# Kernel optimization log

Hardware: AMD Instinct MI355X
Metric: run time of the kernel (lower is better)

The kernel has to match this reference:

```python
import jax, jax.numpy as jnp
import numpy as np

P = 32            # patch_num_row
KS = 5            # kernel_size
DIM = 1024
HEADS = 16
DIM_HEAD = 64
INNER = HEADS * DIM_HEAD
SCALE = DIM_HEAD ** -0.5


def _nearby_mask(p=P, ks=KS):
    # True = masked out (matches torch masked_fill semantics)
    pad = ks // 2
    m = np.ones((p * p, p + 2 * pad, p + 2 * pad), dtype=bool)
    for i in range(p):
        for j in range(p):
            m[i * p + j, i:i + ks, j:j + ks] = False
    m = m[:, pad:-pad, pad:-pad].reshape(p * p, p * p)
    # F.pad(mask, (1,0,1,0), value=False): unmasked first row/col (BOS token)
    m = np.pad(m, ((1, 0), (1, 0)), constant_values=False)
    return jnp.asarray(m)  # [n, n], n = p*p + 1

NB_MASK = _nearby_mask()


def setup_inputs() -> dict:
    key = jax.random.key(0)
    ks = jax.random.split(key, 8)
    b, n = 16, P * P + 1
    s = DIM ** -0.5
    return {
        "q": jax.random.normal(ks[0], (b, n, DIM), jnp.float32),
        "k": jax.random.normal(ks[1], (b, n, DIM), jnp.float32),
        "v": jax.random.normal(ks[2], (b, n, DIM), jnp.float32),
        "Wq": jax.random.normal(ks[3], (DIM, INNER), jnp.float32) * s,
        "Wk": jax.random.normal(ks[4], (DIM, INNER), jnp.float32) * s,
        "Wv": jax.random.normal(ks[5], (DIM, INNER), jnp.float32) * s,
        "Wo": jax.random.normal(ks[6], (INNER, DIM), jnp.float32) * (INNER ** -0.5),
        "bo": jnp.zeros((DIM,), jnp.float32),
    }


def reference(q, k, v, Wq, Wk, Wv, Wo, bo):
    b, n, _ = q.shape
    h, d = HEADS, DIM_HEAD
    # projections, split heads: b n (h d) -> b h n d
    qh = (q @ Wq).reshape(b, n, h, d).transpose(0, 2, 1, 3)
    kh = (k @ Wk).reshape(b, n, h, d).transpose(0, 2, 1, 3)
    vh = (v @ Wv).reshape(b, n, h, d).transpose(0, 2, 1, 3)
    dots = jnp.einsum('bhid,bhjd->bhij', qh, kh) * SCALE
    mask_value = -jnp.finfo(dots.dtype).max
    dots = jnp.where(NB_MASK[None, None], mask_value, dots)
    attn = jax.nn.softmax(dots, axis=-1)
    out = jnp.einsum('bhij,bhjd->bhid', attn, vh)
    out = out.transpose(0, 2, 1, 3).reshape(b, n, h * d)
    return out @ Wo + bo
```

## Files before the change

### kernel.cpp

```cpp
#include <hip/hip_runtime.h>

typedef unsigned short u16;
typedef unsigned int   u32;
typedef __attribute__((ext_vector_type(8))) __bf16 bf16x8;
typedef __attribute__((ext_vector_type(4))) float   f32x4;

#define MROWS 16400
#define NPADROWS 16512
#define KD 1024
#define MATEL ((size_t)NPADROWS * KD)
#define NT 32

__device__ __forceinline__ u16 f2b(float f) {
  union { float f; u32 u; } x; x.f = f;
  return (u16)((x.u + 0x7FFFu + ((x.u >> 16) & 1u)) >> 16);
}
__device__ __forceinline__ float b2f(u16 h) {
  union { u32 u; float f; } x; x.u = ((u32)h) << 16;
  return x.f;
}

__device__ __forceinline__ void gll16(const u16* g, u16* l) {
  __builtin_amdgcn_global_load_lds(
      (const __attribute__((address_space(1))) void*)g,
      (__attribute__((address_space(3))) void*)l, 16, 0, 0);
}

__global__ __launch_bounds__(256) void k_pre(
    const float* __restrict__ W0, const float* __restrict__ W1,
    const float* __restrict__ W2, const float* __restrict__ W3,
    u16* __restrict__ T,
    const float* __restrict__ q, const float* __restrict__ k,
    const float* __restrict__ v, u16* __restrict__ dst)
{
  if (blockIdx.x < 4096) {
    __shared__ float tile[32][33];
    int z = blockIdx.x >> 10;
    int tl = blockIdx.x & 1023;
    int k0 = (tl >> 5) * 32, n0 = (tl & 31) * 32;
    int tx = threadIdx.x & 31, ty = threadIdx.x >> 5;
    const float* W = (z == 0) ? W0 : (z == 1) ? W1 : (z == 2) ? W2 : W3;
    u16* Tz = T + (size_t)z * KD * KD;
#pragma unroll
    for (int r = ty; r < 32; r += 8)
      tile[r][tx] = W[(size_t)(k0 + r) * KD + n0 + tx];
    __syncthreads();
#pragma unroll
    for (int r = ty; r < 32; r += 8)
      Tz[(size_t)(n0 + r) * KD + k0 + tx] = f2b(tile[tx][r]);
  } else {
    int cid = blockIdx.x - 4096;
    const size_t CH_PER_MAT = MATEL / 8;
    const size_t total = 3 * CH_PER_MAT;
    for (size_t c = (size_t)cid * 256 + threadIdx.x; c < total;
         c += (size_t)2048 * 256) {
      size_t z = c / CH_PER_MAT;
      size_t r = c - z * CH_PER_MAT;
      size_t row = r >> 7;
      int col8 = (int)(r & 127) * 8;
      u16* o = dst + z * MATEL + row * KD + col8;
      if (row < MROWS) {
        const float* s = ((z == 0) ? q : (z == 1) ? k : v) + row * KD + col8;
        float4 f0 = *(const float4*)s;
        float4 f1 = *(const float4*)(s + 4);
        ushort4 o0; o0.x = f2b(f0.x); o0.y = f2b(f0.y); o0.z = f2b(f0.z); o0.w = f2b(f0.w);
        ushort4 o1; o1.x = f2b(f1.x); o1.y = f2b(f1.y); o1.z = f2b(f1.z); o1.w = f2b(f1.w);
        *(ushort4*)o = o0; *(ushort4*)(o + 4) = o1;
      } else {
        ushort4 zz; zz.x = zz.y = zz.z = zz.w = 0;
        *(ushort4*)o = zz; *(ushort4*)(o + 4) = zz;
      }
    }
  }
}

template<bool OUT_FP32>
__global__ __launch_bounds__(256) void k_gemm(
    const u16* __restrict__ Ab, const u16* __restrict__ Bt,
    u16* __restrict__ Cb, float* __restrict__ Cf,
    const float* __restrict__ bias, int nwg)
{
  __shared__ u16 lds[2 * 8192];

  int lin = blockIdx.x;
  int cpx = nwg >> 3;
  int swz = (lin & 7) * cpx + (lin >> 3);
  int bn = swz & 7;
  int rest = swz >> 3;
  int bm = rest % 129;
  int z  = rest / 129;

  int t = threadIdx.x;
  int w = t >> 6, l = t & 63;
  int lrow = l & 15, kgrp = l >> 4;
  int wm = (w >> 1) * 64, wn = (w & 1) * 64;

  int srow = w * 16 + (l >> 2);
  int scol = ((l & 3) ^ ((srow >> 1) & 3)) * 8;
  const u16* gA  = Ab + (size_t)z * MATEL + (size_t)(bm * 128 + srow) * KD + scol;
  const u16* gA2 = gA + (size_t)64 * KD;
  const u16* gB  = Bt + (size_t)z * (1024 * 1024) + (size_t)(bn * 128 + srow) * KD + scol;
  const u16* gB2 = gB + (size_t)64 * KD;
  int dA0 = w * 512;
  int dA1 = 2048 + w * 512;
  int dB0 = 4096 + w * 512;
  int dB1 = 6144 + w * 512;

  int qr = (lrow >> 1) & 3;
  int aoff[4], boff[4];
#pragma unroll
  for (int fm = 0; fm < 4; ++fm)
    aoff[fm] = (wm + fm * 16 + lrow) * 32 + ((kgrp ^ qr) * 8);
#pragma unroll
  for (int fn = 0; fn < 4; ++fn)
    boff[fn] = 4096 + (wn + fn * 16 + lrow) * 32 + ((kgrp ^ qr) * 8);

  f32x4 acc[4][4] = {};

#define STAGE(B) { u16* L = lds + (B) * 8192;                         \
    gll16(gA,  L + dA0); gll16(gA2, L + dA1);                         \
    gll16(gB,  L + dB0); gll16(gB2, L + dB1);                         \
    gA += 32; gA2 += 32; gB += 32; gB2 += 32; }

  STAGE(0);
  __syncthreads();

  int buf = 0;
#pragma unroll 2
  for (int kt = 0; kt < NT; ++kt) {
    if (kt + 1 < NT) STAGE(buf ^ 1);

    const u16* Lb = lds + buf * 8192;
    bf16x8 af[4], bfr[4];
#pragma unroll
    for (int fm = 0; fm < 4; ++fm)
      af[fm] = *(const bf16x8*)(Lb + aoff[fm]);
#pragma unroll
    for (int fn = 0; fn < 4; ++fn)
      bfr[fn] = *(const bf16x8*)(Lb + boff[fn]);
#pragma unroll
    for (int fm = 0; fm < 4; ++fm)
#pragma unroll
      for (int fn = 0; fn < 4; ++fn)
        acc[fm][fn] = __builtin_amdgcn_mfma_f32_16x16x32_bf16(af[fm], bfr[fn], acc[fm][fn], 0, 0, 0);

    __syncthreads();
    buf ^= 1;
  }
#undef STAGE

#pragma unroll
  for (int fm = 0; fm < 4; ++fm) {
#pragma unroll
    for (int fn = 0; fn < 4; ++fn) {
      int gcol = bn * 128 + wn + fn * 16 + lrow;
#pragma unroll
      for (int r = 0; r < 4; ++r) {
        int grow = bm * 128 + wm + fm * 16 + kgrp * 4 + r;
        if constexpr (OUT_FP32) {
          if (grow < MROWS)
            Cf[(size_t)grow * KD + gcol] = acc[fm][fn][r] + bias[gcol];
        } else {
          Cb[(size_t)z * MATEL + (size_t)grow * KD + gcol] = f2b(acc[fm][fn][r]);
        }
      }
    }
  }
}

__global__ __launch_bounds__(256) void k_attn(
    const u16* __restrict__ Qp, const u16* __restrict__ Kp,
    const u16* __restrict__ Vp, u16* __restrict__ AO)
{
  int t = threadIdx.x;

  if (blockIdx.x >= 256) {
    __shared__ float sdp[4][16][37];
    __shared__ int   keys[37];
    __shared__ unsigned long long incm[4];

    int bid = blockIdx.x - 256;
    int b = bid >> 8;
    int tile = bid & 255;
    int pi0 = (tile >> 4) * 2, pj0 = (tile & 15) * 2;
    size_t rowbase = (size_t)b * 1025;

    int iq[4];
#pragma unroll
    for (int qi = 0; qi < 4; ++qi)
      iq[qi] = 1 + (pi0 + (qi >> 1)) * 32 + (pj0 + (qi & 1));

    if (t < 37) {
      if (t < 36) {
        int r = pi0 - 2 + t / 6, c = pj0 - 2 + t % 6;
        keys[t] = (r >= 0 && r < 32 && c >= 0 && c < 32) ? (1 + r * 32 + c) : -1;
      } else {
        keys[36] = 0;
      }
    }
    if (t < 4) {
      int di = t >> 1, dj = t & 1;
      unsigned long long m = 1ull << 36;
      for (int j = 0; j < 36; ++j) {
        int wr = j / 6, wc = j % 6;
        if (wr >= di && wr < di + 5 && wc >= dj && wc < dj + 5) m |= 1ull << j;
      }
      incm[t] = m;
    }

    int e = t & 3;
    int hD = (t >> 2) & 15;
    float qreg[4][16];
#pragma unroll
    for (int qi = 0; qi < 4; ++qi) {
      const u16* qp = Qp + (rowbase + iq[qi]) * 1024 + hD * 64 + e * 16;
      uint4 a0 = *(const uint4*)qp;
      uint4 a1 = *(const uint4*)(qp + 8);
      u32 uu[8] = {a0.x, a0.y, a0.z, a0.w, a1.x, a1.y, a1.z, a1.w};
#pragma unroll
      for (int u = 0; u < 8; ++u) {
        qreg[qi][u * 2]     = __uint_as_float(uu[u] << 16);
        qreg[qi][u * 2 + 1] = __uint_as_float(uu[u] & 0xffff0000u);
      }
    }
    __syncthreads();

#pragma unroll
    for (int p = 0; p < 10; ++p) {
      int idx = p * 64 + (t >> 2);
      int j = idx >> 4; if (j > 36) j = 36;
      int key = keys[j];
      int krow = key < 0 ? 0 : key;
      const u16* kp = Kp + (rowbase + krow) * 1024 + hD * 64 + e * 16;
      uint4 kv0 = *(const uint4*)kp;
      uint4 kv1 = *(const uint4*)(kp + 8);
      float s0 = 0.f, s1 = 0.f, s2 = 0.f, s3 = 0.f;
      u32 uu[8] = {kv0.x, kv0.y, kv0.z, kv0.w, kv1.x, kv1.y, kv1.z, kv1.w};
#pragma unroll
      for (int u = 0; u < 8; ++u) {
        float lo = __uint_as_float(uu[u] << 16);
        float hi = __uint_as_float(uu[u] & 0xffff0000u);
        s0 += qreg[0][u * 2] * lo + qreg[0][u * 2 + 1] * hi;
        s1 += qreg[1][u * 2] * lo + qreg[1][u * 2 + 1] * hi;
        s2 += qreg[2][u * 2] * lo + qreg[2][u * 2 + 1] * hi;
        s3 += qreg[3][u * 2] * lo + qreg[3][u * 2 + 1] * hi;
      }
      s0 += __shfl_xor(s0, 1); s0 += __shfl_xor(s0, 2);
      s1 += __shfl_xor(s1, 1); s1 += __shfl_xor(s1, 2);
      s2 += __shfl_xor(s2, 1); s2 += __shfl_xor(s2, 2);
      s3 += __shfl_xor(s3, 1); s3 += __shfl_xor(s3, 2);
      if (idx < 592) {
        float sv = (e == 0) ? s0 : (e == 1) ? s1 : (e == 2) ? s2 : s3;
        sdp[e][hD][j] = (key >= 0) ? sv * 0.125f : -3.0e38f;
      }
    }
    __syncthreads();

    {
      int row = t >> 2;
      int qi = row >> 4, hh = row & 15;
      unsigned long long inc = incm[qi];
      float dv[10];
      float m = -3.0e38f;
#pragma unroll
      for (int s = 0; s < 10; ++s) {
        int j = e + s * 4;
        float d = -3.0e38f;
        if (j < 37) {
          d = sdp[qi][hh][j];
          if (!((inc >> j) & 1)) d = -3.0e38f;
        }
        dv[s] = d;
        m = fmaxf(m, d);
      }
      m = fmaxf(m, __shfl_xor(m, 1));
      m = fmaxf(m, __shfl_xor(m, 2));
      float sum = 0.f;
      float pv[10];
#pragma unroll
      for (int s = 0; s < 10; ++s) {
        int j = e + s * 4;
        float p = (j < 37) ? __expf(dv[s] - m) : 0.f;
        pv[s] = p; sum += p;
      }
      sum += __shfl_xor(sum, 1);
      sum += __shfl_xor(sum, 2);
      float inv = 1.f / sum;
#pragma unroll
      for (int s = 0; s < 10; ++s) {
        int j = e + s * 4;
        if (j < 37) sdp[qi][hh][j] = pv[s] * inv;
      }
    }
    __syncthreads();

    {
      int h = t >> 4;
      int c0 = t * 4;
      float a[4][4] = {};
#pragma unroll 4
      for (int j = 0; j < 37; ++j) {
        int key = keys[j];
        int krow = key < 0 ? 0 : key;
        ushort4 vv = *(const ushort4*)(Vp + (rowbase + krow) * 1024 + c0);
        float v0 = b2f(vv.x), v1 = b2f(vv.y), v2 = b2f(vv.z), v3 = b2f(vv.w);
#pragma unroll
        for (int qi = 0; qi < 4; ++qi) {
          float p = sdp[qi][h][j];
          a[qi][0] += p * v0; a[qi][1] += p * v1;
          a[qi][2] += p * v2; a[qi][3] += p * v3;
        }
      }
#pragma unroll
      for (int qi = 0; qi < 4; ++qi) {
        ushort4 o;
        o.x = f2b(a[qi][0]); o.y = f2b(a[qi][1]);
        o.z = f2b(a[qi][2]); o.w = f2b(a[qi][3]);
        *(ushort4*)&AO[(rowbase + iq[qi]) * 1024 + c0] = o;
      }
    }
  } else {
    __shared__ float q0[64];
    __shared__ float pr[1025];
    __shared__ float red[256];
    __shared__ float red4[256][4];
    int bid = blockIdx.x;
    int b = bid >> 4, h = bid & 15;
    size_t rowbase = (size_t)b * 1025;

    if (t < 64) q0[t] = b2f(Qp[rowbase * 1024 + h * 64 + t]);
    __syncthreads();

    float lmax = -3.0e38f;
    for (int j = t; j < 1025; j += 256) {
      const u16* kp = Kp + (rowbase + j) * 1024 + h * 64;
      float s = 0.f;
#pragma unroll
      for (int e = 0; e < 64; e += 4) {
        ushort4 kv = *(const ushort4*)(kp + e);
        s += q0[e + 0] * b2f(kv.x) + q0[e + 1] * b2f(kv.y)
           + q0[e + 2] * b2f(kv.z) + q0[e + 3] * b2f(kv.w);
      }
      s *= 0.125f;
      pr[j] = s;
      lmax = fmaxf(lmax, s);
    }
    red[t] = lmax; __syncthreads();
    for (int s = 128; s > 0; s >>= 1) {
      if (t < s) red[t] = fmaxf(red[t], red[t + s]);
      __syncthreads();
    }
    float m = red[0]; __syncthreads();

    float lsum = 0.f;
    for (int j = t; j < 1025; j += 256) {
      float p = __expf(pr[j] - m);
      pr[j] = p; lsum += p;
    }
    red[t] = lsum; __syncthreads();
    for (int s = 128; s > 0; s >>= 1) {
      if (t < s) red[t] += red[t + s];
      __syncthreads();
    }
    float inv = 1.f / red[0]; __syncthreads();

    int g16 = t & 15, grp = t >> 4;
    int c0 = h * 64 + g16 * 4;
    float a0 = 0, a1 = 0, a2 = 0, a3 = 0;
    for (int j = grp; j < 1025; j += 16) {
      float p = pr[j];
      ushort4 vv = *(const ushort4*)(Vp + (rowbase + j) * 1024 + c0);
      a0 += p * b2f(vv.x); a1 += p * b2f(vv.y);
      a2 += p * b2f(vv.z); a3 += p * b2f(vv.w);
    }
    red4[t][0] = a0; red4[t][1] = a1; red4[t][2] = a2; red4[t][3] = a3;
    __syncthreads();
    for (int s = 128; s >= 16; s >>= 1) {
      if (t < s) {
#pragma unroll
        for (int kx = 0; kx < 4; ++kx) red4[t][kx] += red4[t + s][kx];
      }
      __syncthreads();
    }
    if (t < 16) {
      ushort4 o;
      o.x = f2b(red4[t][0] * inv); o.y = f2b(red4[t][1] * inv);
      o.z = f2b(red4[t][2] * inv); o.w = f2b(red4[t][3] * inv);
      *(ushort4*)&AO[rowbase * 1024 + h * 64 + t * 4] = o;
    }
  }
}

extern "C" void kernel_launch(void* const* d_in, const int* in_sizes, int n_in,
                              void* d_out, int out_size, void* d_ws, size_t ws_size,
                              hipStream_t stream) {
  const float* q  = (const float*)d_in[0];
  const float* k  = (const float*)d_in[1];
  const float* v  = (const float*)d_in[2];
  const float* Wq = (const float*)d_in[3];
  const float* Wk = (const float*)d_in[4];
  const float* Wv = (const float*)d_in[5];
  const float* Wo = (const float*)d_in[6];
  const float* bo = (const float*)d_in[7];
  float* out = (float*)d_out;

  u16* wt = (u16*)d_ws;
  u16* qb = wt + (size_t)4 * 1024 * 1024;
  u16* Qp = qb + 3 * MATEL;
  u16* Kp = Qp + MATEL;
  u16* Vp = Kp + MATEL;
  u16* AO = qb;

  k_pre<<<6144, 256, 0, stream>>>(Wq, Wk, Wv, Wo, wt, q, k, v, qb);

  k_gemm<false><<<3096, 256, 0, stream>>>(qb, wt, Qp, nullptr, nullptr, 3096);

  k_attn<<<4352, 256, 0, stream>>>(Qp, Kp, Vp, AO);

  k_gemm<true><<<1032, 256, 0, stream>>>(AO, wt + (size_t)3 * 1024 * 1024,
                                         nullptr, out, bo, 1032);
}
```

Before: 355.1 us.

## Use 256x256-tile triple-buffered GEMM for QKV projections

Adds a new GEMM kernel for the Q/K/V projection that uses 256x256 output tiles with 512 threads per workgroup. It triple-buffers LDS via async global-to-LDS loads and interleaves MFMA quadrants with barriers and priority hints. It also remaps workgroups across XCDs in contiguous chunks. Larger tiles raise arithmetic intensity and cut redundant global loads. The trade-off is fewer workgroups (780), higher register and LDS pressure, and tail-tile waste on the 16400-row dimension.

```diff
diff --git a/kernel.cpp b/kernel.cpp
--- a/kernel.cpp
+++ b/kernel.cpp
@@ -75,6 +75,130 @@
 }
 
 template<bool OUT_FP32>
+__global__ __launch_bounds__(512, 1) void k_gemm256(
+    const u16* __restrict__ Ab, const u16* __restrict__ Bt,
+    u16* __restrict__ Cb, float* __restrict__ Cf,
+    const float* __restrict__ bias, int nwg)
+{
+  __shared__ u16 lds[3 * 16384];
+
+  int lin = blockIdx.x;
+  int qq = nwg >> 3, r8 = nwg & 7;
+  int xcd = lin & 7, pos = lin >> 3;
+  int wg = (xcd < r8 ? xcd * (qq + 1) : r8 * (qq + 1) + (xcd - r8) * qq) + pos;
+  int bn = wg & 3;
+  int rest = wg >> 2;
+  int bm = rest % 65;
+  int z  = rest / 65;
+
+  int t = threadIdx.x;
+  int w = t >> 6, l = t & 63;
+  int lrow = l & 15, kgrp = l >> 4;
+  int wrow = w >> 2, wcol = w & 3;
+
+  int pr = t >> 2;
+  int ccl = ((t & 3) ^ ((t >> 3) & 3)) * 8;
+  int ar0 = bm * 256 + pr;        if (ar0 > NPADROWS - 1) ar0 = NPADROWS - 1;
+  int ar1 = bm * 256 + 128 + pr;  if (ar1 > NPADROWS - 1) ar1 = NPADROWS - 1;
+  const u16* gA0 = Ab + (size_t)z * MATEL + (size_t)ar0 * KD + ccl;
+  const u16* gA1 = Ab + (size_t)z * MATEL + (size_t)ar1 * KD + ccl;
+  const u16* gB0 = Bt + (size_t)z * (1024 * 1024) + (size_t)(bn * 256 + pr) * KD + ccl;
+  const u16* gB1 = gB0 + (size_t)128 * KD;
+
+  int qr = (lrow >> 1) & 3;
+  int xk = (kgrp ^ qr) * 8;
+
+  f32x4 acc[8][4] = {};
+  bf16x8 afr[4], bfr2[2];
+
+#define STAGE(B) { u16* L = lds + (B) * 16384;                          \
+    gll16(gA0, L + w * 512);          gll16(gA1, L + 4096 + w * 512);   \
+    gll16(gB0, L + 8192 + w * 512);   gll16(gB1, L + 12288 + w * 512);  \
+    gA0 += 32; gA1 += 32; gB0 += 32; gB1 += 32; }
+
+#define WAITV4 do { __builtin_amdgcn_sched_barrier(0);                  \
+    asm volatile("s_waitcnt vmcnt(4)" ::: "memory");                    \
+    __builtin_amdgcn_sched_barrier(0); } while (0)
+#define WAITV0 do { __builtin_amdgcn_sched_barrier(0);                  \
+    asm volatile("s_waitcnt vmcnt(0)" ::: "memory");                    \
+    __builtin_amdgcn_sched_barrier(0); } while (0)
+#define BAR do { __builtin_amdgcn_sched_barrier(0);                     \
+    __builtin_amdgcn_s_barrier();                                       \
+    __builtin_amdgcn_sched_barrier(0); } while (0)
+
+#define READ_A(FM0) {                                                   \
+    _Pragma("unroll")                                                   \
+    for (int qa = 0; qa < 4; ++qa)                                      \
+      afr[qa] = *(const bf16x8*)(Lb + (wrow * 128 + (FM0 + qa) * 16 + lrow) * 32 + xk); }
+#define READ_B(FN0) {                                                   \
+    _Pragma("unroll")                                                   \
+    for (int qb = 0; qb < 2; ++qb)                                      \
+      bfr2[qb] = *(const bf16x8*)(Lb + 8192 + (wcol * 64 + (FN0 + qb) * 16 + lrow) * 32 + xk); }
+#define MFMA_Q(FM0, FN0) {                                              \
+    __builtin_amdgcn_s_setprio(1);                                      \
+    _Pragma("unroll")                                                   \
+    for (int qa = 0; qa < 4; ++qa)                                      \
+      _Pragma("unroll")                                                 \
+      for (int qb = 0; qb < 2; ++qb)                                    \
+        acc[FM0 + qa][FN0 + qb] = __builtin_amdgcn_mfma_f32_16x16x32_bf16( \
+            afr[qa], bfr2[qb], acc[FM0 + qa][FN0 + qb], 0, 0, 0);       \
+    __builtin_amdgcn_s_setprio(0); }
+
+  STAGE(0); STAGE(1);
+  WAITV4;
+  BAR;
+
+  int cur = 0;
+  for (int kt = 0; kt < NT; ++kt) {
+    if (kt + 2 < NT) {
+      int pre = cur + 2; if (pre >= 3) pre -= 3;
+      STAGE(pre);
+    }
+    const u16* Lb = lds + cur * 16384;
+    READ_A(0); READ_B(0);
+    BAR; MFMA_Q(0, 0); BAR;
+    READ_B(2);
+    BAR; MFMA_Q(0, 2); BAR;
+    READ_A(4);
+    BAR; MFMA_Q(4, 2); BAR;
+    READ_B(0);
+    BAR; MFMA_Q(4, 0);
+    if (kt + 1 < NT) {
+      if (kt + 2 < NT) { WAITV4; }
+      else            { WAITV0; }
+      BAR;
+    }
+    cur += 1; if (cur == 3) cur = 0;
+  }
+#undef STAGE
+#undef WAITV4
+#undef WAITV0
+#undef BAR
+#undef READ_A
+#undef READ_B
+#undef MFMA_Q
+
+#pragma unroll
+  for (int fm = 0; fm < 8; ++fm) {
+#pragma unroll
+    for (int fn = 0; fn < 4; ++fn) {
+      int gcol = bn * 256 + wcol * 64 + fn * 16 + lrow;
+#pragma unroll
+      for (int r = 0; r < 4; ++r) {
+        int grow = bm * 256 + wrow * 128 + fm * 16 + kgrp * 4 + r;
+        if constexpr (OUT_FP32) {
+          if (grow < MROWS)
+            Cf[(size_t)grow * KD + gcol] = acc[fm][fn][r] + bias[gcol];
+        } else {
+          if (grow < NPADROWS)
+            Cb[(size_t)z * MATEL + (size_t)grow * KD + gcol] = f2b(acc[fm][fn][r]);
+        }
+      }
+    }
+  }
+}
+
+template<bool OUT_FP32>
 __global__ __launch_bounds__(256) void k_gemm(
     const u16* __restrict__ Ab, const u16* __restrict__ Bt,
     u16* __restrict__ Cb, float* __restrict__ Cf,
@@ -413,7 +537,7 @@
 
   k_pre<<<6144, 256, 0, stream>>>(Wq, Wk, Wv, Wo, wt, q, k, v, qb);
 
-  k_gemm<false><<<3096, 256, 0, stream>>>(qb, wt, Qp, nullptr, nullptr, 3096);
+  k_gemm256<false><<<780, 512, 0, stream>>>(qb, wt, Qp, nullptr, nullptr, 780);
 
   k_attn<<<4352, 256, 0, stream>>>(Qp, Kp, Vp, AO);
 
```

Result: no change. 350.0 us (-1.4%).
